# Optimization experiments

Measured on AMD Instinct MI355X. Metric: run time of the kernel, lower is better.

Reference implementation:

```python
import jax, jax.numpy as jnp
import numpy as np

LENGTH = 5
TOP_K = 5
POOL_SIZE = 60
EMBED_DIM = 768
MAP_SCALE = 0.1
MAX_NORM = 1.0 - 4e-3  # Poincare ball projection eps for float32 (geoopt convention)
EPS = 1e-12


def _l2_normalize(x):
    ss = jnp.sum(x * x, axis=-1, keepdims=True)
    return x * jax.lax.rsqrt(jnp.maximum(ss, EPS))


def _expmap0(u):
    # c = 1: expmap0(u) = tanh(||u||) * u / ||u||
    n = jnp.sqrt(jnp.maximum(jnp.sum(u * u, axis=-1, keepdims=True), 1e-15))
    return jnp.tanh(n) * u / n


def _proju0(x):
    # project onto the open unit ball
    n = jnp.sqrt(jnp.maximum(jnp.sum(x * x, axis=-1, keepdims=True), 1e-15))
    return jnp.where(n > MAX_NORM, x * (MAX_NORM / n), x)


def _map_to_ball(x):
    return _proju0(_expmap0(_l2_normalize(x) * MAP_SCALE))


def _mobius_add(x, y):
    # c = 1 Mobius addition, broadcasting over leading dims
    x2 = jnp.sum(x * x, axis=-1, keepdims=True)
    y2 = jnp.sum(y * y, axis=-1, keepdims=True)
    xy = jnp.sum(x * y, axis=-1, keepdims=True)
    num = (1.0 + 2.0 * xy + y2) * x + (1.0 - x2) * y
    den = 1.0 + 2.0 * xy + x2 * y2
    return num / jnp.maximum(den, 1e-15)


def _poincare_dist(x, y):
    # dist(x, y) = 2 * artanh(||(-x) mobius+ y||)  (c = 1)
    d = _mobius_add(-x, y)
    n = jnp.sqrt(jnp.maximum(jnp.sum(d * d, axis=-1), 1e-15))
    n = jnp.clip(n, 0.0, 1.0 - 1e-7)
    return 2.0 * jnp.arctanh(n)


def setup_inputs() -> dict:
    key = jax.random.key(0)
    k1, k2, k3 = jax.random.split(key, 3)
    x_embed = jax.random.normal(k1, (128, 512, EMBED_DIM), dtype=jnp.float32)
    prompt = jax.random.uniform(k2, (POOL_SIZE, LENGTH, EMBED_DIM), dtype=jnp.float32, minval=-1.0, maxval=1.0)
    prompt_key = jax.random.uniform(k3, (POOL_SIZE, EMBED_DIM), dtype=jnp.float32, minval=-1.0, maxval=1.0)
    return {"x_embed": x_embed, "prompt": prompt, "prompt_key": prompt_key}


def reference(x_embed, prompt, prompt_key):
    B = x_embed.shape[0]
    x_mean = jnp.mean(x_embed, axis=1)                      # [B, D]
    key_ball = _map_to_ball(prompt_key)                     # [P, D]
    q_ball = _map_to_ball(x_mean)                           # [B, D]
    dist = _poincare_dist(q_ball[:, None, :], key_ball[None, :, :])  # [B, P]
    similarity = -dist
    _, idx = jax.lax.top_k(similarity, TOP_K)               # [B, K]
    idx = jnp.sort(idx, axis=1)
    batched_prompt = prompt[idx].reshape(B, TOP_K * LENGTH, EMBED_DIM)
    selected_key = key_ball[idx]                            # [B, K, D]
    selected_dist = jnp.take_along_axis(dist, idx, axis=1)  # [B, K]
    reduce_sim = jnp.sum(selected_dist) / B
    prompted_embedding = jnp.concatenate([batched_prompt, x_embed], axis=1)
    return (prompted_embedding, reduce_sim, idx, similarity, selected_key)
```

## Files before the change

kernel.cpp:

```cpp
#include <hip/hip_runtime.h>

#define EMBED   768
#define EMBED4  192
#define POOL    60
#define BATCH   128
#define SEQ     512
#define TOPK    5
#define LEN     5
#define OUTROWS 537

#define SZ_PE   (128L*537L*768L)
#define OFF_RS  (SZ_PE)
#define OFF_IDX (OFF_RS + 1)
#define OFF_SIM (OFF_IDX + 640)
#define OFF_SK  (OFF_SIM + 7680)

#define WS_PARTIAL 0
#define WS_MEAN    393216
#define WS_KEYBALL 491520
#define WS_KEYY2   537600
#define WS_IDX     537664

#define MAX_NORM_F 0.996f

__device__ __forceinline__ float block_reduce_256(float v, float* red) {
    int tid = threadIdx.x;
    #pragma unroll
    for (int m = 32; m >= 1; m >>= 1) v += __shfl_xor(v, m, 64);
    if ((tid & 63) == 0) red[tid >> 6] = v;
    __syncthreads();
    float total = red[0] + red[1] + red[2] + red[3];
    __syncthreads();
    return total;
}

__global__ __launch_bounds__(192) void mean_partial_copy(
        const float* __restrict__ x, float* __restrict__ out, float* __restrict__ partial) {
    const int slice = blockIdx.x, b = blockIdx.y, tid = threadIdx.x;
    const float4* __restrict__ x4 = (const float4*)x;
    float4* __restrict__ out4 = (float4*)out;
    float4* __restrict__ p4 = (float4*)partial;

    float4 acc = make_float4(0.f, 0.f, 0.f, 0.f);
    const long srow = (long)b * SEQ + slice * 128;
    const long obase = ((long)b * OUTROWS + 25 + slice * 128) * EMBED4 + tid;
    const long ibase = srow * EMBED4 + tid;
    for (int s = 0; s < 128; ++s) {
        float4 v = x4[ibase + (long)s * EMBED4];
        acc.x += v.x; acc.y += v.y; acc.z += v.z; acc.w += v.w;
        out4[obase + (long)s * EMBED4] = v;
    }
    p4[(long)(b * 4 + slice) * EMBED4 + tid] = acc;
}

__global__ __launch_bounds__(192) void finalize_mean(
        const float* __restrict__ partial, float* __restrict__ mean) {
    const int b = blockIdx.x, tid = threadIdx.x;
    const float4* __restrict__ p4 = (const float4*)partial;
    float4* __restrict__ m4 = (float4*)mean;
    float4 a = p4[(b * 4 + 0) * EMBED4 + tid];
    float4 c = p4[(b * 4 + 1) * EMBED4 + tid];
    float4 d = p4[(b * 4 + 2) * EMBED4 + tid];
    float4 e = p4[(b * 4 + 3) * EMBED4 + tid];
    const float inv = 1.0f / 512.0f;
    float4 r;
    r.x = (a.x + c.x + d.x + e.x) * inv;
    r.y = (a.y + c.y + d.y + e.y) * inv;
    r.z = (a.z + c.z + d.z + e.z) * inv;
    r.w = (a.w + c.w + d.w + e.w) * inv;
    m4[b * EMBED4 + tid] = r;
}

__global__ __launch_bounds__(256) void keyball_kernel(
        const float* __restrict__ pkey, float* __restrict__ keyball, float* __restrict__ keyy2) {
    __shared__ float red[4];
    const int p = blockIdx.x, tid = threadIdx.x;
    float v[3];
    float ss = 0.f;
    #pragma unroll
    for (int j = 0; j < 3; ++j) { v[j] = pkey[p * EMBED + tid + 256 * j]; ss += v[j] * v[j]; }
    ss = block_reduce_256(ss, red);
    const float scale1 = rsqrtf(fmaxf(ss, 1e-12f)) * 0.1f;
    float su = 0.f;
    #pragma unroll
    for (int j = 0; j < 3; ++j) { v[j] *= scale1; su += v[j] * v[j]; }
    su = block_reduce_256(su, red);
    const float n = sqrtf(fmaxf(su, 1e-15f));
    const float f = tanhf(n) / n;
    float sb = 0.f;
    #pragma unroll
    for (int j = 0; j < 3; ++j) { v[j] *= f; sb += v[j] * v[j]; }
    sb = block_reduce_256(sb, red);
    const float n2 = sqrtf(fmaxf(sb, 1e-15f));
    const float g = (n2 > MAX_NORM_F) ? (MAX_NORM_F / n2) : 1.0f;
    #pragma unroll
    for (int j = 0; j < 3; ++j) keyball[p * EMBED + tid + 256 * j] = v[j] * g;
    if (tid == 0) keyy2[p] = sb * g * g;
}

__global__ __launch_bounds__(256) void topk_kernel(
        const float* __restrict__ mean, const float* __restrict__ keyball,
        const float* __restrict__ keyy2, float* __restrict__ out, int* __restrict__ idxws) {
    __shared__ float red[4];
    __shared__ float q[EMBED];
    __shared__ float xy[POOL];
    __shared__ float dist[POOL];
    __shared__ int sel_sh[TOPK];
    const int b = blockIdx.x, tid = threadIdx.x;

    float v[3];
    float ss = 0.f;
    #pragma unroll
    for (int j = 0; j < 3; ++j) { v[j] = mean[b * EMBED + tid + 256 * j]; ss += v[j] * v[j]; }
    ss = block_reduce_256(ss, red);
    const float scale1 = rsqrtf(fmaxf(ss, 1e-12f)) * 0.1f;
    float su = 0.f;
    #pragma unroll
    for (int j = 0; j < 3; ++j) { v[j] *= scale1; su += v[j] * v[j]; }
    su = block_reduce_256(su, red);
    const float n = sqrtf(fmaxf(su, 1e-15f));
    const float f = tanhf(n) / n;
    float sb = 0.f;
    #pragma unroll
    for (int j = 0; j < 3; ++j) { v[j] *= f; sb += v[j] * v[j]; }
    sb = block_reduce_256(sb, red);
    const float n2 = sqrtf(fmaxf(sb, 1e-15f));
    const float g = (n2 > MAX_NORM_F) ? (MAX_NORM_F / n2) : 1.0f;
    const float x2 = sb * g * g;
    #pragma unroll
    for (int j = 0; j < 3; ++j) q[tid + 256 * j] = v[j] * g;
    __syncthreads();

    const int wave = tid >> 6, lane = tid & 63;
    for (int p = wave; p < POOL; p += 4) {
        const float* __restrict__ kb = keyball + p * EMBED;
        float acc = 0.f;
        #pragma unroll
        for (int d = 0; d < EMBED; d += 64) acc += q[d + lane] * kb[d + lane];
        #pragma unroll
        for (int m = 32; m >= 1; m >>= 1) acc += __shfl_xor(acc, m, 64);
        if (lane == 0) xy[p] = acc;
    }
    __syncthreads();

    if (tid < POOL) {
        const float s = xy[tid];
        const float y2 = keyy2[tid];
        const float A = 1.0f - 2.0f * s + y2;
        const float B = 1.0f - x2;
        const float num2 = A * A * x2 + B * B * y2 - 2.0f * A * B * s;
        const float den = fmaxf(1.0f - 2.0f * s + x2 * y2, 1e-15f);
        float nn = sqrtf(fmaxf(num2 / (den * den), 1e-15f));
        nn = fminf(fmaxf(nn, 0.0f), 1.0f - 1e-7f);
        const float dd = logf((1.0f + nn) / (1.0f - nn));
        dist[tid] = dd;
        out[OFF_SIM + (long)b * POOL + tid] = -dd;
    }
    __syncthreads();

    if (tid == 0) {
        int sel[TOPK];
        unsigned long long mask = 0ULL;
        for (int k = 0; k < TOPK; ++k) {
            int best = 0; float bd = 1e30f;
            for (int p = 0; p < POOL; ++p) {
                if (mask & (1ULL << p)) continue;
                if (dist[p] < bd) { bd = dist[p]; best = p; }
            }
            mask |= 1ULL << best;
            sel[k] = best;
        }
        #pragma unroll
        for (int i = 0; i < TOPK; ++i)
            for (int j2 = i + 1; j2 < TOPK; ++j2)
                if (sel[j2] < sel[i]) { int t = sel[i]; sel[i] = sel[j2]; sel[j2] = t; }
        float sum = 0.f;
        for (int k = 0; k < TOPK; ++k) {
            sum += dist[sel[k]];
            out[OFF_IDX + (long)b * TOPK + k] = (float)sel[k];
            idxws[b * TOPK + k] = sel[k];
            sel_sh[k] = sel[k];
        }
        atomicAdd(&out[OFF_RS], sum * (1.0f / 128.0f));
    }
    __syncthreads();

    for (int t = tid; t < TOPK * EMBED; t += 256) {
        const int k = t / EMBED, d = t - k * EMBED;
        out[OFF_SK + (long)b * TOPK * EMBED + t] = keyball[sel_sh[k] * EMBED + d];
    }
}

__global__ __launch_bounds__(192) void prompt_copy(
        const float* __restrict__ prompt, const int* __restrict__ idxws, float* __restrict__ out) {
    const int r = blockIdx.x, b = blockIdx.y, tid = threadIdx.x;
    const int k = r / LEN, l = r - k * LEN;
    const int pi = idxws[b * TOPK + k];
    const float4* __restrict__ p4 = (const float4*)prompt;
    float4* __restrict__ o4 = (float4*)out;
    o4[((long)b * OUTROWS + r) * EMBED4 + tid] = p4[((long)pi * LEN + l) * EMBED4 + tid];
}

extern "C" void kernel_launch(void* const* d_in, const int* in_sizes, int n_in,
                              void* d_out, int out_size, void* d_ws, size_t ws_size,
                              hipStream_t stream) {
    const float* x      = (const float*)d_in[0];
    const float* prompt = (const float*)d_in[1];
    const float* pkey   = (const float*)d_in[2];
    float* out = (float*)d_out;
    float* ws  = (float*)d_ws;

    float* partial = ws + WS_PARTIAL;
    float* mean    = ws + WS_MEAN;
    float* keyball = ws + WS_KEYBALL;
    float* keyy2   = ws + WS_KEYY2;
    int*   idxws   = (int*)(ws + WS_IDX);

    hipMemsetAsync(out + OFF_RS, 0, sizeof(float), stream);

    hipLaunchKernelGGL(mean_partial_copy, dim3(4, 128), dim3(192), 0, stream, x, out, partial);
    hipLaunchKernelGGL(finalize_mean,     dim3(128),    dim3(192), 0, stream, partial, mean);
    hipLaunchKernelGGL(keyball_kernel,    dim3(60),     dim3(256), 0, stream, pkey, keyball, keyy2);
    hipLaunchKernelGGL(topk_kernel,       dim3(128),    dim3(256), 0, stream, mean, keyball, keyy2, out, idxws);
    hipLaunchKernelGGL(prompt_copy,       dim3(25, 128), dim3(192), 0, stream, prompt, idxws, out);
}
```

Baseline: 401.3 us.

## Raise mean slice parallelism and fuse finalize and prompt copy into topk kernel

Splits the streaming mean/copy kernel into 16 slices per batch instead of 4, giving 2048 blocks rather than 512 so more memory requests are in flight for the dominant ~400MB copy. The finalize_mean and prompt_copy kernels are folded into the topk kernel, which now sums the 16 partials itself and copies the selected prompt rows directly. The memset is replaced by an in-kernel zero write. This cuts launch count, at the cost of a longer serial tail in the 128-block topk kernel, which now also does the prompt gather.

```diff
diff --git a/kernel.cpp b/kernel.cpp
--- a/kernel.cpp
+++ b/kernel.cpp
@@ -8,6 +8,7 @@
 #define TOPK    5
 #define LEN     5
 #define OUTROWS 537
+#define NSLICE  16
 
 #define SZ_PE   (128L*537L*768L)
 #define OFF_RS  (SZ_PE)
@@ -16,10 +17,8 @@
 #define OFF_SK  (OFF_SIM + 7680)
 
 #define WS_PARTIAL 0
-#define WS_MEAN    393216
-#define WS_KEYBALL 491520
-#define WS_KEYY2   537600
-#define WS_IDX     537664
+#define WS_KEYBALL 1572864
+#define WS_KEYY2   1618944
 
 #define MAX_NORM_F 0.996f
 
@@ -41,34 +40,19 @@
     float4* __restrict__ out4 = (float4*)out;
     float4* __restrict__ p4 = (float4*)partial;
 
+    if (slice == 0 && b == 0 && tid == 0) out[OFF_RS] = 0.0f;
+
     float4 acc = make_float4(0.f, 0.f, 0.f, 0.f);
-    const long srow = (long)b * SEQ + slice * 128;
-    const long obase = ((long)b * OUTROWS + 25 + slice * 128) * EMBED4 + tid;
-    const long ibase = srow * EMBED4 + tid;
-    for (int s = 0; s < 128; ++s) {
+    const int rows = SEQ / NSLICE;
+    const long ibase = ((long)b * SEQ + slice * rows) * EMBED4 + tid;
+    const long obase = ((long)b * OUTROWS + 25 + slice * rows) * EMBED4 + tid;
+    #pragma unroll 4
+    for (int s = 0; s < rows; ++s) {
         float4 v = x4[ibase + (long)s * EMBED4];
         acc.x += v.x; acc.y += v.y; acc.z += v.z; acc.w += v.w;
         out4[obase + (long)s * EMBED4] = v;
     }
-    p4[(long)(b * 4 + slice) * EMBED4 + tid] = acc;
-}
-
-__global__ __launch_bounds__(192) void finalize_mean(
-        const float* __restrict__ partial, float* __restrict__ mean) {
-    const int b = blockIdx.x, tid = threadIdx.x;
-    const float4* __restrict__ p4 = (const float4*)partial;
-    float4* __restrict__ m4 = (float4*)mean;
-    float4 a = p4[(b * 4 + 0) * EMBED4 + tid];
-    float4 c = p4[(b * 4 + 1) * EMBED4 + tid];
-    float4 d = p4[(b * 4 + 2) * EMBED4 + tid];
-    float4 e = p4[(b * 4 + 3) * EMBED4 + tid];
-    const float inv = 1.0f / 512.0f;
-    float4 r;
-    r.x = (a.x + c.x + d.x + e.x) * inv;
-    r.y = (a.y + c.y + d.y + e.y) * inv;
-    r.z = (a.z + c.z + d.z + e.z) * inv;
-    r.w = (a.w + c.w + d.w + e.w) * inv;
-    m4[b * EMBED4 + tid] = r;
+    p4[(long)(b * NSLICE + slice) * EMBED4 + tid] = acc;
 }
 
 __global__ __launch_bounds__(256) void keyball_kernel(
@@ -98,9 +82,10 @@
     if (tid == 0) keyy2[p] = sb * g * g;
 }
 
-__global__ __launch_bounds__(256) void topk_kernel(
-        const float* __restrict__ mean, const float* __restrict__ keyball,
-        const float* __restrict__ keyy2, float* __restrict__ out, int* __restrict__ idxws) {
+__global__ __launch_bounds__(256) void topk_fused(
+        const float* __restrict__ partial, const float* __restrict__ keyball,
+        const float* __restrict__ keyy2, const float* __restrict__ prompt,
+        float* __restrict__ out) {
     __shared__ float red[4];
     __shared__ float q[EMBED];
     __shared__ float xy[POOL];
@@ -109,9 +94,22 @@
     const int b = blockIdx.x, tid = threadIdx.x;
 
     float v[3];
+    {
+        const float inv = 1.0f / (float)SEQ;
+        #pragma unroll
+        for (int j = 0; j < 3; ++j) {
+            const int col = tid + 256 * j;
+            float s = 0.f;
+            #pragma unroll
+            for (int sl = 0; sl < NSLICE; ++sl)
+                s += partial[(long)(b * NSLICE + sl) * EMBED + col];
+            v[j] = s * inv;
+        }
+    }
+
     float ss = 0.f;
     #pragma unroll
-    for (int j = 0; j < 3; ++j) { v[j] = mean[b * EMBED + tid + 256 * j]; ss += v[j] * v[j]; }
+    for (int j = 0; j < 3; ++j) ss += v[j] * v[j];
     ss = block_reduce_256(ss, red);
     const float scale1 = rsqrtf(fmaxf(ss, 1e-12f)) * 0.1f;
     float su = 0.f;
@@ -178,7 +176,6 @@
         for (int k = 0; k < TOPK; ++k) {
             sum += dist[sel[k]];
             out[OFF_IDX + (long)b * TOPK + k] = (float)sel[k];
-            idxws[b * TOPK + k] = sel[k];
             sel_sh[k] = sel[k];
         }
         atomicAdd(&out[OFF_RS], sum * (1.0f / 128.0f));
@@ -189,16 +186,17 @@
         const int k = t / EMBED, d = t - k * EMBED;
         out[OFF_SK + (long)b * TOPK * EMBED + t] = keyball[sel_sh[k] * EMBED + d];
     }
-}
-
-__global__ __launch_bounds__(192) void prompt_copy(
-        const float* __restrict__ prompt, const int* __restrict__ idxws, float* __restrict__ out) {
-    const int r = blockIdx.x, b = blockIdx.y, tid = threadIdx.x;
-    const int k = r / LEN, l = r - k * LEN;
-    const int pi = idxws[b * TOPK + k];
-    const float4* __restrict__ p4 = (const float4*)prompt;
-    float4* __restrict__ o4 = (float4*)out;
-    o4[((long)b * OUTROWS + r) * EMBED4 + tid] = p4[((long)pi * LEN + l) * EMBED4 + tid];
+
+    {
+        const float4* __restrict__ p4 = (const float4*)prompt;
+        float4* __restrict__ o4 = (float4*)out;
+        for (int t = tid; t < TOPK * LEN * EMBED4; t += 256) {
+            const int r = t / EMBED4, c = t - r * EMBED4;
+            const int k = r / LEN, l = r - k * LEN;
+            const int pi = sel_sh[k];
+            o4[((long)b * OUTROWS + r) * EMBED4 + c] = p4[((long)pi * LEN + l) * EMBED4 + c];
+        }
+    }
 }
 
 extern "C" void kernel_launch(void* const* d_in, const int* in_sizes, int n_in,
@@ -211,16 +209,11 @@
     float* ws  = (float*)d_ws;
 
     float* partial = ws + WS_PARTIAL;
-    float* mean    = ws + WS_MEAN;
     float* keyball = ws + WS_KEYBALL;
     float* keyy2   = ws + WS_KEYY2;
-    int*   idxws   = (int*)(ws + WS_IDX);
-
-    hipMemsetAsync(out + OFF_RS, 0, sizeof(float), stream);
-
-    hipLaunchKernelGGL(mean_partial_copy, dim3(4, 128), dim3(192), 0, stream, x, out, partial);
-    hipLaunchKernelGGL(finalize_mean,     dim3(128),    dim3(192), 0, stream, partial, mean);
-    hipLaunchKernelGGL(keyball_kernel,    dim3(60),     dim3(256), 0, stream, pkey, keyball, keyy2);
-    hipLaunchKernelGGL(topk_kernel,       dim3(128),    dim3(256), 0, stream, mean, keyball, keyy2, out, idxws);
-    hipLaunchKernelGGL(prompt_copy,       dim3(25, 128), dim3(192), 0, stream, prompt, idxws, out);
-}
+
+    hipLaunchKernelGGL(mean_partial_copy, dim3(NSLICE, 128), dim3(192), 0, stream, x, out, partial);
+    hipLaunchKernelGGL(keyball_kernel,    dim3(60),          dim3(256), 0, stream, pkey, keyball, keyy2);
+    hipLaunchKernelGGL(topk_fused,        dim3(128),         dim3(256), 0, stream,
+                       partial, keyball, keyy2, prompt, out);
+}
```

New measurement: 392.8 us. 2.1% less time.
